# Performance work log

Hardware: AMD Instinct MI355X
Metric: run time of the kernel (lower is better)

The kernel has to match this reference:

```python
import jax, jax.numpy as jnp
import numpy as np

MODES1 = 12
MODES2 = 12
IN_CH = 32
OUT_CH = 32
B, H, W = 16, 256, 256
SCALE = 1.0 / (IN_CH * OUT_CH)


def setup_inputs() -> dict:
    key = jax.random.key(0)
    k1, k2, k3 = jax.random.split(key, 3)
    x = jax.random.normal(k1, (B, IN_CH, H, W), dtype=jnp.float32)
    w1 = SCALE * jax.random.uniform(k2, (IN_CH, OUT_CH, MODES1, MODES2, 2), dtype=jnp.float32)
    w2 = SCALE * jax.random.uniform(k3, (IN_CH, OUT_CH, MODES1, MODES2, 2), dtype=jnp.float32)
    return {"x": x, "weights1": w1, "weights2": w2}


def _compl_mul2d(inp, w):
    # inp: [b,i,x,y] complex ; w: [i,o,x,y,2] real -> complex
    wc = jax.lax.complex(w[..., 0], w[..., 1])
    return jnp.einsum('bixy,ioxy->boxy', inp, wc)


def reference(x, weights1, weights2):
    H_, W_ = x.shape[-2], x.shape[-1]
    m1 = min(MODES1, H_ // 2)
    m2 = min(MODES2, W_ // 2 + 1)
    x_ft = jnp.fft.rfft2(x.astype(jnp.float32))  # [B, Cin, H, W//2+1]
    low = _compl_mul2d(x_ft[:, :, :m1, :m2], weights1[:, :, :m1, :m2])
    high = _compl_mul2d(x_ft[:, :, -m1:, :m2], weights2[:, :, :m1, :m2])
    out_ft = jnp.zeros((x.shape[0], OUT_CH, H_, W_ // 2 + 1), dtype=jnp.complex64)
    out_ft = out_ft.at[:, :, :m1, :m2].set(low)
    out_ft = out_ft.at[:, :, H_ - m1:, :m2].set(high)
    return jnp.fft.irfft2(out_ft, s=(H_, W_)).astype(x.dtype)
```

## Files before the change

### kernel.cpp

```cpp
#include <hip/hip_runtime.h>


#define TPI 6.28318530717958647692f

__global__ __launch_bounds__(256, 2) void k12_hwdft(const float* __restrict__ x,
                                                    float* __restrict__ Xf) {
  __shared__ float2 step2[64];
  __shared__ float red[4 * 7 * 128];
  __shared__ float2 Ys2[13 * 129];
  const int blk = blockIdx.x;
  const int bi = blk >> 1, wh = blk & 1;
  const int t = threadIdx.x;
  const int q = t >> 6, l = t & 63;

  if (t < 64) {
    float s, c;
    sincosf(TPI * (float)t * (1.0f / 256.0f), &s, &c);
    step2[t] = make_float2(c, s);
  }
  __syncthreads();

  const float2* xp2 = reinterpret_cast<const float2*>(x + (size_t)bi * 65536 + wh * 128) + l;
  float2 aC[13], aS12[12];
#pragma unroll
  for (int j = 0; j < 13; j++) aC[j] = make_float2(0.f, 0.f);
#pragma unroll
  for (int j = 0; j < 12; j++) aS12[j] = make_float2(0.f, 0.f);

  const int h0 = q * 16;
#pragma unroll 2
  for (int hh = 0; hh < 16; hh++) {
    int h = h0 + hh;
    float2 x0 = xp2[h * 128];
    float2 x1 = xp2[(h + 64) * 128];
    float2 x2 = xp2[(h + 128) * 128];
    float2 x3 = xp2[(h + 192) * 128];
    float2 p02 = make_float2(x0.x + x2.x, x0.y + x2.y);
    float2 m02 = make_float2(x0.x - x2.x, x0.y - x2.y);
    float2 p13 = make_float2(x1.x + x3.x, x1.y + x3.y);
    float2 m13 = make_float2(x1.x - x3.x, x1.y - x3.y);
    float2 A = make_float2(p02.x + p13.x, p02.y + p13.y);
    float2 Bv = make_float2(p02.x - p13.x, p02.y - p13.y);
    aC[0].x += A.x; aC[0].y += A.y;
    float2 st = step2[h];
    float cj = st.x, sj = st.y;
#pragma unroll
    for (int jj = 0; jj < 12; jj++) {
      const int j = jj + 1, r = j & 3;
      if (r == 0) {
        aC[j].x = fmaf(A.x, cj, aC[j].x);   aC[j].y = fmaf(A.y, cj, aC[j].y);
        aS12[jj].x = fmaf(A.x, sj, aS12[jj].x); aS12[jj].y = fmaf(A.y, sj, aS12[jj].y);
      } else if (r == 2) {
        aC[j].x = fmaf(Bv.x, cj, aC[j].x);  aC[j].y = fmaf(Bv.y, cj, aC[j].y);
        aS12[jj].x = fmaf(Bv.x, sj, aS12[jj].x); aS12[jj].y = fmaf(Bv.y, sj, aS12[jj].y);
      } else if (r == 1) {
        aC[j].x = fmaf(m02.x, cj, fmaf(-m13.x, sj, aC[j].x));
        aC[j].y = fmaf(m02.y, cj, fmaf(-m13.y, sj, aC[j].y));
        aS12[jj].x = fmaf(m02.x, sj, fmaf(m13.x, cj, aS12[jj].x));
        aS12[jj].y = fmaf(m02.y, sj, fmaf(m13.y, cj, aS12[jj].y));
      } else {
        aC[j].x = fmaf(m02.x, cj, fmaf(m13.x, sj, aC[j].x));
        aC[j].y = fmaf(m02.y, cj, fmaf(m13.y, sj, aC[j].y));
        aS12[jj].x = fmaf(m02.x, sj, fmaf(-m13.x, cj, aS12[jj].x));
        aS12[jj].y = fmaf(m02.y, sj, fmaf(-m13.y, cj, aS12[jj].y));
      }
      if (jj < 11) {
        float nc = fmaf(cj, st.x, -(sj * st.y));
        float ns = fmaf(cj, st.y, sj * st.x);
        cj = nc; sj = ns;
      }
    }
  }

  for (int p = 0; p < 4; p++) {
    __syncthreads();
#pragma unroll
    for (int cc = 0; cc < 7; cc++) {
      int cls = p * 7 + cc;
      if (cls < 26) {
        int j = cls >> 1;
        float2 v;
        if (cls & 1) v = (j == 0) ? make_float2(0.f, 0.f) : aS12[j - 1];
        else v = aC[j];
        *reinterpret_cast<float2*>(&red[(q * 7 + cc) * 128 + 2 * l]) = v;
      }
    }
    __syncthreads();
    for (int idx = t; idx < 7 * 128; idx += 256) {
      int cc = idx >> 7, wl = idx & 127;
      int cls = p * 7 + cc;
      if (cls < 26) {
        float s = red[(0 * 7 + cc) * 128 + wl] + red[(1 * 7 + cc) * 128 + wl] +
                  red[(2 * 7 + cc) * 128 + wl] + red[(3 * 7 + cc) * 128 + wl];
        if (cls & 1) Ys2[(cls >> 1) * 129 + wl].y = s;
        else         Ys2[(cls >> 1) * 129 + wl].x = s;
      }
    }
  }
  __syncthreads();

  if (t < 156) {
    int j = t / 12, kx = t % 12;
    float cs, ss;
    {
      float s, c;
      sincosf(TPI * (float)kx * (1.0f / 256.0f), &s, &c);
      cs = c; ss = -s;
    }
    const float2* CS = &Ys2[j * 129];
    float pr = 1.0f, pi = 0.0f;
    float A = 0, B = 0, D = 0, E = 0;
#pragma unroll 4
    for (int w = 0; w < 128; w++) {
      float2 v = CS[w];
      A = fmaf(v.x, pr, A);
      B = fmaf(v.x, pi, B);
      D = fmaf(v.y, pr, D);
      E = fmaf(v.y, pi, E);
      float npr = pr * cs - pi * ss;
      float npi = pr * ss + pi * cs;
      pr = npr; pi = npi;
    }
    float sgn = (wh && (kx & 1)) ? -1.0f : 1.0f;
    A *= sgn; B *= sgn; D *= sgn; E *= sgn;
    float2* Xo = reinterpret_cast<float2*>(Xf) + (size_t)wh * 147456;
    size_t base = (size_t)kx * 512 + bi;
    if (j <= 11) Xo[(size_t)j * 6144 + base] = make_float2(A + E, B - D);
    if (j >= 1)  Xo[(size_t)(24 - j) * 6144 + base] = make_float2(A - E, B + D);
  }
}

__global__ __launch_bounds__(256) void k3_mix(const float* __restrict__ Xf,
                                              const float* __restrict__ w1,
                                              const float* __restrict__ w2,
                                              float* __restrict__ Ff) {
  __shared__ float Xs[1024];
  __shared__ float Ws[2048];
  int m = blockIdx.x;
  int ky = m / 12, kx = m % 12;
  int t = threadIdx.x;
  const float* Xsl = Xf + (size_t)m * 1024;
  for (int e = t; e < 1024; e += 256) Xs[e] = Xsl[e] + Xsl[e + 294912];
  const float* Wp = (ky < 12) ? w1 : w2;
  int myr = (ky < 12) ? ky : ky - 12;
  int woff = myr * 24 + kx * 2;
  for (int e = t; e < 1024; e += 256) {
    float2 wv = *reinterpret_cast<const float2*>(Wp + (size_t)e * 288 + woff);
    Ws[e * 2] = wv.x; Ws[e * 2 + 1] = wv.y;
  }
  __syncthreads();
  int o = t & 31, bh = t >> 5;
  float ar = 0, ai = 0, br = 0, bi_ = 0;
#pragma unroll
  for (int i = 0; i < 32; i++) {
    float wr = Ws[i * 64 + o * 2], wi = Ws[i * 64 + o * 2 + 1];
    float x1r = Xs[bh * 64 + i * 2], x1i = Xs[bh * 64 + i * 2 + 1];
    float x2r = Xs[(bh + 8) * 64 + i * 2], x2i = Xs[(bh + 8) * 64 + i * 2 + 1];
    ar = fmaf(x1r, wr, ar); ar = fmaf(-x1i, wi, ar);
    ai = fmaf(x1r, wi, ai); ai = fmaf(x1i, wr, ai);
    br = fmaf(x2r, wr, br); br = fmaf(-x2i, wi, br);
    bi_ = fmaf(x2r, wi, bi_); bi_ = fmaf(x2i, wr, bi_);
  }
  float scale = (kx == 0 ? 1.0f : 2.0f) * (1.0f / 65536.0f);
  float2* Fo = reinterpret_cast<float2*>(Ff) + (size_t)m * 512;
  Fo[(size_t)bh * 32 + o] = make_float2(ar * scale, ai * scale);
  Fo[(size_t)(bh + 8) * 32 + o] = make_float2(br * scale, bi_ * scale);
}

__global__ __launch_bounds__(256) void k45_inv(const float* __restrict__ Ff,
                                               float* __restrict__ out) {
  __shared__ float tw[128 * 27];
  __shared__ float PQ[13 * 12 * 4];
  __shared__ float Gs[256 * 24];
  const int bo = blockIdx.x;
  const int t = threadIdx.x;
  const int l = t & 63, wq = t >> 6;

  for (int e = t; e < 128 * 13; e += 256) {
    int h = e / 13, j = e % 13;
    float s, c;
    sincosf(TPI * (float)((h * j) & 255) * (1.0f / 256.0f), &s, &c);
    tw[h * 27 + 2 * j] = c;
    tw[h * 27 + 2 * j + 1] = s;
  }
  if (t < 156) {
    int j = t / 12, kx = t % 12;
    const float2* F2 = reinterpret_cast<const float2*>(Ff);
    float lr = 0, li = 0, hr = 0, hi = 0;
    if (j < 12) { float2 v = F2[((size_t)j * 12 + kx) * 512 + bo]; lr = v.x; li = v.y; }
    if (j > 0)  { float2 v = F2[((size_t)(24 - j) * 12 + kx) * 512 + bo]; hr = v.x; hi = v.y; }
    PQ[(j * 12 + kx) * 4 + 0] = lr + hr;
    PQ[(j * 12 + kx) * 4 + 1] = li + hi;
    PQ[(j * 12 + kx) * 4 + 2] = hi - li;
    PQ[(j * 12 + kx) * 4 + 3] = lr - hr;
  }
  __syncthreads();

  if (t < 192) {
    const int kx = t % 12, hq = t / 12;
    float Pr[13], Pi[13], Qr[13], Qi[13];
#pragma unroll
    for (int j = 0; j < 13; j++) {
      Pr[j] = PQ[(j * 12 + kx) * 4 + 0];
      Pi[j] = PQ[(j * 12 + kx) * 4 + 1];
      Qr[j] = PQ[(j * 12 + kx) * 4 + 2];
      Qi[j] = PQ[(j * 12 + kx) * 4 + 3];
    }
    for (int hh = 0; hh < 8; hh++) {
      int h = hh * 16 + hq;
      float Er = 0, Ei = 0, Or = 0, Oi = 0;
#pragma unroll
      for (int j = 0; j < 13; j++) {
        float c = tw[h * 27 + 2 * j], s = tw[h * 27 + 2 * j + 1];
        if (j & 1) {
          Or = fmaf(Pr[j], c, Or); Or = fmaf(Qr[j], s, Or);
          Oi = fmaf(Pi[j], c, Oi); Oi = fmaf(Qi[j], s, Oi);
        } else {
          Er = fmaf(Pr[j], c, Er); Er = fmaf(Qr[j], s, Er);
          Ei = fmaf(Pi[j], c, Ei); Ei = fmaf(Qi[j], s, Ei);
        }
      }
      Gs[h * 24 + 2 * kx] = Er + Or;
      Gs[h * 24 + 2 * kx + 1] = Ei + Oi;
      Gs[(h + 128) * 24 + 2 * kx] = Er - Or;
      Gs[(h + 128) * 24 + 2 * kx + 1] = Ei - Oi;
    }
  }

  float cA[12], sA[12], cB[12], sB[12];
#pragma unroll
  for (int kx = 1; kx < 12; kx++) {
    float s, c;
    __sincosf(TPI * (float)((kx * (2 * l)) & 255) * (1.0f / 256.0f), &s, &c);
    cA[kx] = c; sA[kx] = s;
    __sincosf(TPI * (float)((kx * (2 * l + 1)) & 255) * (1.0f / 256.0f), &s, &c);
    cB[kx] = c; sB[kx] = s;
  }
  __syncthreads();

  float* ob0 = out + ((size_t)bo * 256 + wq * 64) * 256;
  for (int rs = 0; rs < 64; rs++) {
    int rl = wq * 64 + rs;
    float g[24];
    const float4* gr4 = reinterpret_cast<const float4*>(&Gs[rl * 24]);
#pragma unroll
    for (int qq = 0; qq < 6; qq++) {
      float4 v = gr4[qq];
      g[4 * qq] = v.x; g[4 * qq + 1] = v.y; g[4 * qq + 2] = v.z; g[4 * qq + 3] = v.w;
    }
    float E0 = g[0], O0 = 0, E1 = g[0], O1 = 0;
#pragma unroll
    for (int kx = 1; kx < 12; kx++) {
      float ta = g[2 * kx] * cA[kx] - g[2 * kx + 1] * sA[kx];
      float tb = g[2 * kx] * cB[kx] - g[2 * kx + 1] * sB[kx];
      if (kx & 1) { O0 += ta; O1 += tb; } else { E0 += ta; E1 += tb; }
    }
    float* orow = ob0 + rs * 256;
    *reinterpret_cast<float2*>(&orow[2 * l]) = make_float2(E0 + O0, E1 + O1);
    *reinterpret_cast<float2*>(&orow[128 + 2 * l]) = make_float2(E0 - O0, E1 - O1);
  }
}

extern "C" void kernel_launch(void* const* d_in, const int* in_sizes, int n_in,
                              void* d_out, int out_size, void* d_ws, size_t ws_size,
                              hipStream_t stream) {
  const float* x = (const float*)d_in[0];
  const float* w1 = (const float*)d_in[1];
  const float* w2 = (const float*)d_in[2];
  float* out = (float*)d_out;
  float* ws = (float*)d_ws;

  float* Xf = ws;
  float* Ff = ws + 589824;

  k12_hwdft<<<1024, 256, 0, stream>>>(x, Xf);
  k3_mix<<<288, 256, 0, stream>>>(Xf, w1, w2, Ff);
  k45_inv<<<512, 256, 0, stream>>>(Ff, out);
}
```

Baseline: 77.89 us.

## Process full 256-wide image per block with float4 loads, drop half-split merge

The forward DFT kernel now handles a whole 256-column image per block, loading float4 per thread, instead of splitting each image into two 128-column halves across two blocks. This removes the second partial-spectrum buffer and the extra add in the mixing kernel, and halves the grid to 512 blocks. In exchange, each thread keeps twice as many accumulator registers (float4 instead of float2), shared memory roughly doubles, and the W-direction DFT loop runs 256 iterations per thread, which may cut occupancy and lengthen the serial tail.

```diff
diff --git a/kernel.cpp b/kernel.cpp
--- a/kernel.cpp
+++ b/kernel.cpp
@@ -6,10 +6,9 @@
 __global__ __launch_bounds__(256, 2) void k12_hwdft(const float* __restrict__ x,
                                                     float* __restrict__ Xf) {
   __shared__ float2 step2[64];
-  __shared__ float red[4 * 7 * 128];
-  __shared__ float2 Ys2[13 * 129];
-  const int blk = blockIdx.x;
-  const int bi = blk >> 1, wh = blk & 1;
+  __shared__ float red[4 * 7 * 256];
+  __shared__ float2 Ys2[13 * 257];
+  const int bi = blockIdx.x;
   const int t = threadIdx.x;
   const int q = t >> 6, l = t & 63;
 
@@ -20,49 +19,60 @@
   }
   __syncthreads();
 
-  const float2* xp2 = reinterpret_cast<const float2*>(x + (size_t)bi * 65536 + wh * 128) + l;
-  float2 aC[13], aS12[12];
-#pragma unroll
-  for (int j = 0; j < 13; j++) aC[j] = make_float2(0.f, 0.f);
-#pragma unroll
-  for (int j = 0; j < 12; j++) aS12[j] = make_float2(0.f, 0.f);
-
-  const int h0 = q * 16;
+  const float4* xp4 = reinterpret_cast<const float4*>(x + (size_t)bi * 65536) + l;
+  float4 aC[13], aS12[12];
+#pragma unroll
+  for (int j = 0; j < 13; j++) aC[j] = make_float4(0.f, 0.f, 0.f, 0.f);
+#pragma unroll
+  for (int j = 0; j < 12; j++) aS12[j] = make_float4(0.f, 0.f, 0.f, 0.f);
+
 #pragma unroll 2
-  for (int hh = 0; hh < 16; hh++) {
-    int h = h0 + hh;
-    float2 x0 = xp2[h * 128];
-    float2 x1 = xp2[(h + 64) * 128];
-    float2 x2 = xp2[(h + 128) * 128];
-    float2 x3 = xp2[(h + 192) * 128];
-    float2 p02 = make_float2(x0.x + x2.x, x0.y + x2.y);
-    float2 m02 = make_float2(x0.x - x2.x, x0.y - x2.y);
-    float2 p13 = make_float2(x1.x + x3.x, x1.y + x3.y);
-    float2 m13 = make_float2(x1.x - x3.x, x1.y - x3.y);
-    float2 A = make_float2(p02.x + p13.x, p02.y + p13.y);
-    float2 Bv = make_float2(p02.x - p13.x, p02.y - p13.y);
-    aC[0].x += A.x; aC[0].y += A.y;
+  for (int i = 0; i < 16; i++) {
+    const int h = 4 * i + q;
+    float4 x0 = xp4[h * 64];
+    float4 x1 = xp4[(h + 64) * 64];
+    float4 x2 = xp4[(h + 128) * 64];
+    float4 x3 = xp4[(h + 192) * 64];
+    float4 p02 = make_float4(x0.x + x2.x, x0.y + x2.y, x0.z + x2.z, x0.w + x2.w);
+    float4 m02 = make_float4(x0.x - x2.x, x0.y - x2.y, x0.z - x2.z, x0.w - x2.w);
+    float4 p13 = make_float4(x1.x + x3.x, x1.y + x3.y, x1.z + x3.z, x1.w + x3.w);
+    float4 m13 = make_float4(x1.x - x3.x, x1.y - x3.y, x1.z - x3.z, x1.w - x3.w);
+    float4 A = make_float4(p02.x + p13.x, p02.y + p13.y, p02.z + p13.z, p02.w + p13.w);
+    float4 Bv = make_float4(p02.x - p13.x, p02.y - p13.y, p02.z - p13.z, p02.w - p13.w);
+    aC[0].x += A.x; aC[0].y += A.y; aC[0].z += A.z; aC[0].w += A.w;
     float2 st = step2[h];
     float cj = st.x, sj = st.y;
 #pragma unroll
     for (int jj = 0; jj < 12; jj++) {
       const int j = jj + 1, r = j & 3;
       if (r == 0) {
-        aC[j].x = fmaf(A.x, cj, aC[j].x);   aC[j].y = fmaf(A.y, cj, aC[j].y);
+        aC[j].x = fmaf(A.x, cj, aC[j].x); aC[j].y = fmaf(A.y, cj, aC[j].y);
+        aC[j].z = fmaf(A.z, cj, aC[j].z); aC[j].w = fmaf(A.w, cj, aC[j].w);
         aS12[jj].x = fmaf(A.x, sj, aS12[jj].x); aS12[jj].y = fmaf(A.y, sj, aS12[jj].y);
+        aS12[jj].z = fmaf(A.z, sj, aS12[jj].z); aS12[jj].w = fmaf(A.w, sj, aS12[jj].w);
       } else if (r == 2) {
-        aC[j].x = fmaf(Bv.x, cj, aC[j].x);  aC[j].y = fmaf(Bv.y, cj, aC[j].y);
+        aC[j].x = fmaf(Bv.x, cj, aC[j].x); aC[j].y = fmaf(Bv.y, cj, aC[j].y);
+        aC[j].z = fmaf(Bv.z, cj, aC[j].z); aC[j].w = fmaf(Bv.w, cj, aC[j].w);
         aS12[jj].x = fmaf(Bv.x, sj, aS12[jj].x); aS12[jj].y = fmaf(Bv.y, sj, aS12[jj].y);
+        aS12[jj].z = fmaf(Bv.z, sj, aS12[jj].z); aS12[jj].w = fmaf(Bv.w, sj, aS12[jj].w);
       } else if (r == 1) {
         aC[j].x = fmaf(m02.x, cj, fmaf(-m13.x, sj, aC[j].x));
         aC[j].y = fmaf(m02.y, cj, fmaf(-m13.y, sj, aC[j].y));
+        aC[j].z = fmaf(m02.z, cj, fmaf(-m13.z, sj, aC[j].z));
+        aC[j].w = fmaf(m02.w, cj, fmaf(-m13.w, sj, aC[j].w));
         aS12[jj].x = fmaf(m02.x, sj, fmaf(m13.x, cj, aS12[jj].x));
         aS12[jj].y = fmaf(m02.y, sj, fmaf(m13.y, cj, aS12[jj].y));
+        aS12[jj].z = fmaf(m02.z, sj, fmaf(m13.z, cj, aS12[jj].z));
+        aS12[jj].w = fmaf(m02.w, sj, fmaf(m13.w, cj, aS12[jj].w));
       } else {
         aC[j].x = fmaf(m02.x, cj, fmaf(m13.x, sj, aC[j].x));
         aC[j].y = fmaf(m02.y, cj, fmaf(m13.y, sj, aC[j].y));
+        aC[j].z = fmaf(m02.z, cj, fmaf(m13.z, sj, aC[j].z));
+        aC[j].w = fmaf(m02.w, cj, fmaf(m13.w, sj, aC[j].w));
         aS12[jj].x = fmaf(m02.x, sj, fmaf(-m13.x, cj, aS12[jj].x));
         aS12[jj].y = fmaf(m02.y, sj, fmaf(-m13.y, cj, aS12[jj].y));
+        aS12[jj].z = fmaf(m02.z, sj, fmaf(-m13.z, cj, aS12[jj].z));
+        aS12[jj].w = fmaf(m02.w, sj, fmaf(-m13.w, cj, aS12[jj].w));
       }
       if (jj < 11) {
         float nc = fmaf(cj, st.x, -(sj * st.y));
@@ -79,21 +89,21 @@
       int cls = p * 7 + cc;
       if (cls < 26) {
         int j = cls >> 1;
-        float2 v;
-        if (cls & 1) v = (j == 0) ? make_float2(0.f, 0.f) : aS12[j - 1];
+        float4 v;
+        if (cls & 1) v = (j == 0) ? make_float4(0.f, 0.f, 0.f, 0.f) : aS12[j - 1];
         else v = aC[j];
-        *reinterpret_cast<float2*>(&red[(q * 7 + cc) * 128 + 2 * l]) = v;
+        *reinterpret_cast<float4*>(&red[(q * 7 + cc) * 256 + 4 * l]) = v;
       }
     }
     __syncthreads();
-    for (int idx = t; idx < 7 * 128; idx += 256) {
-      int cc = idx >> 7, wl = idx & 127;
+    for (int idx = t; idx < 7 * 256; idx += 256) {
+      int cc = idx >> 8, wl = idx & 255;
       int cls = p * 7 + cc;
       if (cls < 26) {
-        float s = red[(0 * 7 + cc) * 128 + wl] + red[(1 * 7 + cc) * 128 + wl] +
-                  red[(2 * 7 + cc) * 128 + wl] + red[(3 * 7 + cc) * 128 + wl];
-        if (cls & 1) Ys2[(cls >> 1) * 129 + wl].y = s;
-        else         Ys2[(cls >> 1) * 129 + wl].x = s;
+        float s = red[(0 * 7 + cc) * 256 + wl] + red[(1 * 7 + cc) * 256 + wl] +
+                  red[(2 * 7 + cc) * 256 + wl] + red[(3 * 7 + cc) * 256 + wl];
+        if (cls & 1) Ys2[(cls >> 1) * 257 + wl].y = s;
+        else         Ys2[(cls >> 1) * 257 + wl].x = s;
       }
     }
   }
@@ -107,11 +117,11 @@
       sincosf(TPI * (float)kx * (1.0f / 256.0f), &s, &c);
       cs = c; ss = -s;
     }
-    const float2* CS = &Ys2[j * 129];
+    const float2* CS = &Ys2[j * 257];
     float pr = 1.0f, pi = 0.0f;
     float A = 0, B = 0, D = 0, E = 0;
 #pragma unroll 4
-    for (int w = 0; w < 128; w++) {
+    for (int w = 0; w < 256; w++) {
       float2 v = CS[w];
       A = fmaf(v.x, pr, A);
       B = fmaf(v.x, pi, B);
@@ -121,9 +131,7 @@
       float npi = pr * ss + pi * cs;
       pr = npr; pi = npi;
     }
-    float sgn = (wh && (kx & 1)) ? -1.0f : 1.0f;
-    A *= sgn; B *= sgn; D *= sgn; E *= sgn;
-    float2* Xo = reinterpret_cast<float2*>(Xf) + (size_t)wh * 147456;
+    float2* Xo = reinterpret_cast<float2*>(Xf);
     size_t base = (size_t)kx * 512 + bi;
     if (j <= 11) Xo[(size_t)j * 6144 + base] = make_float2(A + E, B - D);
     if (j >= 1)  Xo[(size_t)(24 - j) * 6144 + base] = make_float2(A - E, B + D);
@@ -140,7 +148,7 @@
   int ky = m / 12, kx = m % 12;
   int t = threadIdx.x;
   const float* Xsl = Xf + (size_t)m * 1024;
-  for (int e = t; e < 1024; e += 256) Xs[e] = Xsl[e] + Xsl[e + 294912];
+  for (int e = t; e < 1024; e += 256) Xs[e] = Xsl[e];
   const float* Wp = (ky < 12) ? w1 : w2;
   int myr = (ky < 12) ? ky : ky - 12;
   int woff = myr * 24 + kx * 2;
@@ -271,9 +279,9 @@
   float* ws = (float*)d_ws;
 
   float* Xf = ws;
-  float* Ff = ws + 589824;
-
-  k12_hwdft<<<1024, 256, 0, stream>>>(x, Xf);
+  float* Ff = ws + 294912;
+
+  k12_hwdft<<<512, 256, 0, stream>>>(x, Xf);
   k3_mix<<<288, 256, 0, stream>>>(Xf, w1, w2, Ff);
   k45_inv<<<512, 256, 0, stream>>>(Ff, out);
 }
```

New measurement: 78.46 us. About the same (+0.7%).
